# Optimization experiments

Hardware: AMD Instinct MI355X
Metric: run time of the kernel (lower is better)

The kernel has to match this reference:

```python
import jax, jax.numpy as jnp
import numpy as np

B, C1, C2, H, W, NH = 16, 256, 256, 64, 64, 8
C = C2 // 2          # hidden dim of retention blocks (c2*e)
HD = C // NH         # head dim
EPS = 1e-5           # torch BatchNorm2d / LayerNorm default eps


def _ln(x, g, b):
    mu = jnp.mean(x, -1, keepdims=True)
    var = jnp.mean((x - mu) ** 2, -1, keepdims=True)
    return (x - mu) * jax.lax.rsqrt(var + EPS) * g + b


def _bn_silu(y, g, b, m, v):
    # inference-mode BatchNorm2d (running stats) + SiLU, channels axis=1
    y = (y - m[:, None, None]) * jax.lax.rsqrt(v + EPS)[:, None, None] * g[:, None, None] + b[:, None, None]
    return jax.nn.silu(y)


def _decay1d(L, dec):
    # RelPos2d.generate_1d_decay: exp(decay_n * |i-j|), shape (NH, L, L)
    idx = jnp.arange(L)
    m = jnp.abs(idx[:, None] - idx[None, :]).astype(jnp.float32)
    return jnp.exp(dec[:, None, None] * m)


def setup_inputs() -> dict:
    key = jax.random.key(0)
    ks = jax.random.split(key, 8)
    s = 0.02
    return {
        'x': jax.random.normal(ks[0], (B, C1, H, W), jnp.float32),
        'cv1_w': jax.random.normal(ks[1], (2 * C, C1), jnp.float32) * s,
        'bn1_g': jnp.ones((2 * C,)), 'bn1_b': jnp.zeros((2 * C,)),
        'bn1_m': jnp.zeros((2 * C,)), 'bn1_v': jnp.ones((2 * C,)),
        'cv2_w': jax.random.normal(ks[2], (C2, 3 * C), jnp.float32) * s,
        'bn2_g': jnp.ones((C2,)), 'bn2_b': jnp.zeros((C2,)),
        'bn2_m': jnp.zeros((C2,)), 'bn2_v': jnp.ones((C2,)),
        'ln1_g': jnp.ones((C,)), 'ln1_b': jnp.zeros((C,)),
        'qkv_w': jax.random.normal(ks[3], (3 * C, C), jnp.float32) * s,
        'qkv_b': jnp.zeros((3 * C,)),
        'proj_w': jax.random.normal(ks[4], (C, C), jnp.float32) * s,
        'proj_b': jnp.zeros((C,)),
        'gamma': jnp.ones((C,)),
        'ln2_g': jnp.ones((C,)), 'ln2_b': jnp.zeros((C,)),
        'ffn_w1': jax.random.normal(ks[5], (2 * C, C), jnp.float32) * s,
        'ffn_b1': jnp.zeros((2 * C,)),
        'ffn_w2': jax.random.normal(ks[6], (C, 2 * C), jnp.float32) * s,
        'ffn_b2': jnp.zeros((C,)),
    }


def reference(x, cv1_w, bn1_g, bn1_b, bn1_m, bn1_v, cv2_w, bn2_g, bn2_b, bn2_m, bn2_v,
              ln1_g, ln1_b, qkv_w, qkv_b, proj_w, proj_b, gamma,
              ln2_g, ln2_b, ffn_w1, ffn_b1, ffn_w2, ffn_b2):
    # RelPos2d: decay per head, initial_value=2, heads_range=4; mode='chunk' -> 1D decays
    dec = jnp.log(1.0 - 2.0 ** (-2.0 - 4.0 * jnp.arange(NH, dtype=jnp.float32) / NH))
    decay_h = _decay1d(H, dec)  # (NH, H, H)
    decay_w = _decay1d(W, dec)  # (NH, W, W)

    # cv1: 1x1 conv + BN + SiLU, then chunk into two halves of C channels
    y = _bn_silu(jnp.einsum('bchw,oc->bohw', x, cv1_w), bn1_g, bn1_b, bn1_m, bn1_v)
    y1, y2 = y[:, :C], y[:, C:]

    # RetBlock on channels-last feature map
    f = jnp.transpose(y2, (0, 2, 3, 1))  # (B,H,W,C)
    res = f
    fn = _ln(f, ln1_g, ln1_b)
    qkv = fn @ qkv_w.T + qkv_b
    q, k, v = jnp.split(qkv, 3, axis=-1)

    def heads(t):
        return jnp.transpose(t.reshape(B, H, W, NH, HD), (0, 3, 1, 2, 4))  # (B,NH,H,W,HD)

    q, k, v = heads(q), heads(k), heads(v)

    # axial retention: row attention with exponential row-decay
    qk_h = jnp.einsum('bnhwc,bnHwc->bnhHw', q, k) * decay_h[None, :, :, :, None]
    out_h = jnp.einsum('bnhHw,bnHwc->bnhwc', qk_h, v)
    # column attention with exponential column-decay
    qk_w = jnp.einsum('bnhwc,bnhWc->bnhwW', q, k) * decay_w[None, :, None, :, :]
    out_w = jnp.einsum('bnhwW,bnhWc->bnhwc', qk_w, v)
    out = 0.5 * (out_h + out_w)
    out = jnp.transpose(out, (0, 2, 3, 1, 4)).reshape(B, H, W, C)

    f = res + (out @ proj_w.T + proj_b) * gamma
    res2 = f
    fn2 = _ln(f, ln2_g, ln2_b)
    h1 = jax.nn.gelu(fn2 @ ffn_w1.T + ffn_b1, approximate=False)
    f = res2 + (h1 @ ffn_w2.T + ffn_b2)

    f = jnp.transpose(f, (0, 3, 1, 2))  # back to (B,C,H,W)
    cat = jnp.concatenate([y1, y2, f], axis=1)  # (B,3C,H,W)
    return _bn_silu(jnp.einsum('bchw,oc->bohw', cat, cv2_w), bn2_g, bn2_b, bn2_m, bn2_v)
```

## Files before the change

kernel.cpp:

```cpp
#include <hip/hip_runtime.h>
#include <math.h>

#define LEPS 1e-5f
static constexpr int NPOS = 65536;

typedef __attribute__((ext_vector_type(8))) short short8;
typedef __attribute__((ext_vector_type(4))) float floatx4;

__device__ __forceinline__ ushort f2bf(float f) {
    unsigned int u = __float_as_uint(f);
    u += 0x7FFF + ((u >> 16) & 1);
    return (ushort)(u >> 16);
}
__device__ __forceinline__ float bfu(ushort h) {
    return __uint_as_float((unsigned int)h << 16);
}
__device__ __forceinline__ float bfl(unsigned int u) {
    return __uint_as_float(u << 16);
}
__device__ __forceinline__ float bfh(unsigned int u) {
    return __uint_as_float(u & 0xffff0000u);
}

struct WcvtArgs { const float* src[6]; ushort* dst[6]; int n[6]; };
__global__ __launch_bounds__(256)
void wcvt_k(WcvtArgs a)
{
    const int seg = blockIdx.y;
    const float* s = a.src[seg];
    ushort* d = a.dst[seg];
    const int n = a.n[seg];
    for (int i = blockIdx.x * 256 + threadIdx.x; i < n; i += gridDim.x * 256)
        d[i] = f2bf(s[i]);
}

__global__ __launch_bounds__(256)
void bnprep_k(const float* g1, const float* b1, const float* m1, const float* v1,
              const float* g2, const float* b2, const float* m2, const float* v2,
              float* s1, float* h1, float* s2, float* h2)
{
    const int i = threadIdx.x;
    if (blockIdx.x == 0) {
        const float s = g1[i] * rsqrtf(v1[i] + LEPS);
        s1[i] = s; h1[i] = b1[i] - m1[i] * s;
    } else {
        const float s = g2[i] * rsqrtf(v2[i] + LEPS);
        s2[i] = s; h2[i] = b2[i] - m2[i] * s;
    }
}

__global__ __launch_bounds__(256)
void tr_k(const float* __restrict__ x, ushort* __restrict__ xT)
{
    __shared__ float tile[64][65];
    const int t = threadIdx.x;
    const int bi = blockIdx.x;
    const int hwt = bi & 63, ct = (bi >> 6) & 3, b = bi >> 8;
    const int p0 = b * 4096 + hwt * 64, c0 = ct * 64;
    const float* src = x + ((size_t)(b * 256 + c0) << 12) + hwt * 64;
#pragma unroll
    for (int i = 0; i < 16; i++) {
        int cc = (t >> 6) + i * 4;
        tile[cc][t & 63] = src[((size_t)cc << 12) + (t & 63)];
    }
    __syncthreads();
    const int c2 = (t & 31) * 2;
    const int pr = t >> 5;
#pragma unroll
    for (int i = 0; i < 8; i++) {
        int pp = pr + i * 8;
        unsigned int u = (unsigned int)f2bf(tile[c2][pp])
                       | ((unsigned int)f2bf(tile[c2 + 1][pp]) << 16);
        *(unsigned int*)&xT[(size_t)(p0 + pp) * 256 + c0 + c2] = u;
    }
}

template<int KDIM, int ARS, int AMODE, int EPI, int LN>
__global__ __launch_bounds__(256)
void gemm_k(const ushort* __restrict__ A0, const ushort* __restrict__ A1,
            const ushort* __restrict__ Wm, const float* __restrict__ bias,
            const float* __restrict__ q0, const float* __restrict__ q1,
            const ushort* __restrict__ resh,
            const float* __restrict__ lng, const float* __restrict__ lnb,
            ushort* __restrict__ lnout, void* __restrict__ outv, int ors)
{
    __shared__ __align__(16) ushort smem[2 * 128 * 72];
    ushort (*As)[72] = (ushort (*)[72])smem;
    ushort (*Bs)[72] = (ushort (*)[72])(smem + 128 * 72);
    const int t = threadIdx.x;
    const int p0 = blockIdx.x * 128;
    const int o0 = blockIdx.y * 128;
    const int row = t >> 1, half = t & 1;
    const int lane = t & 63, wv = t >> 6;
    const int wm = (wv & 1) * 64, wn = (wv >> 1) * 64;
    const int ln15 = lane & 15, quad = lane >> 4;
    floatx4 acc[4][4] = {};

    for (int k0 = 0; k0 < KDIM; k0 += 64) {
        if (AMODE == 3) {
            const ushort* s1 = A0 + (size_t)(p0 + row) * 128 + k0 + half * 32;
            const ushort* s2 = A1 + (size_t)(p0 + row) * 128 + k0 + half * 32;
#pragma unroll
            for (int i = 0; i < 4; i++) {
                uint4 ua = ((const uint4*)s1)[i];
                uint4 ub = ((const uint4*)s2)[i];
                const unsigned int* ap = (const unsigned int*)&ua;
                const unsigned int* bp = (const unsigned int*)&ub;
                uint4 w;
                unsigned int* wp = (unsigned int*)&w;
#pragma unroll
                for (int j = 0; j < 4; j++)
                    wp[j] = (unsigned int)f2bf(0.5f * (bfl(ap[j]) + bfl(bp[j])))
                          | ((unsigned int)f2bf(0.5f * (bfh(ap[j]) + bfh(bp[j]))) << 16);
                *(uint4*)&As[row][half * 32 + i * 8] = w;
            }
        } else {
            const ushort* s;
            if (AMODE == 2) {
                if (k0 < 256) s = A0 + (size_t)(p0 + row) * 256 + k0 + half * 32;
                else          s = A1 + (size_t)(p0 + row) * 128 + (k0 - 256) + half * 32;
            } else {
                s = A0 + (size_t)(p0 + row) * ARS + k0 + half * 32;
            }
#pragma unroll
            for (int i = 0; i < 4; i++)
                *(uint4*)&As[row][half * 32 + i * 8] = ((const uint4*)s)[i];
        }
        {
            const ushort* s = Wm + (size_t)(o0 + row) * KDIM + k0 + half * 32;
#pragma unroll
            for (int i = 0; i < 4; i++)
                *(uint4*)&Bs[row][half * 32 + i * 8] = ((const uint4*)s)[i];
        }
        __syncthreads();
#pragma unroll
        for (int kc = 0; kc < 64; kc += 32) {
            short8 a[4], b[4];
#pragma unroll
            for (int i = 0; i < 4; i++)
                a[i] = *(const short8*)&As[wm + i * 16 + ln15][kc + quad * 8];
#pragma unroll
            for (int j = 0; j < 4; j++)
                b[j] = *(const short8*)&Bs[wn + j * 16 + ln15][kc + quad * 8];
#pragma unroll
            for (int i = 0; i < 4; i++)
#pragma unroll
                for (int j = 0; j < 4; j++)
                    acc[i][j] = __builtin_amdgcn_mfma_f32_16x16x32_bf16(
                        a[i], b[j], acc[i][j], 0, 0, 0);
        }
        __syncthreads();
    }

    if (EPI == 2) {
        float* cb = (float*)smem;
        float* ob = (float*)outv + (((size_t)(p0 >> 12) * 256) << 12);
        const int hw0 = p0 & 4095;
#pragma unroll
        for (int chunk = 0; chunk < 2; chunk++) {
            __syncthreads();
            if ((wn >> 6) == chunk) {
#pragma unroll
                for (int i = 0; i < 4; i++)
#pragma unroll
                for (int j = 0; j < 4; j++) {
                    const int ch = j * 16 + ln15;
                    const int o = o0 + chunk * 64 + ch;
                    const float sc = q0[o], sh = q1[o];
#pragma unroll
                    for (int r = 0; r < 4; r++) {
                        const int pos = wm + i * 16 + quad * 4 + r;
                        float v = acc[i][j][r] * sc + sh;
                        v = v / (1.f + __expf(-v));
                        cb[ch * 132 + pos] = v;
                    }
                }
            }
            __syncthreads();
#pragma unroll
            for (int it = 0; it < 8; it++) {
                const int flat = it * 1024 + t * 4;
                const int ch = flat >> 7, pos = flat & 127;
                const int o = o0 + chunk * 64 + ch;
                float4 v4 = *(const float4*)&cb[ch * 132 + pos];
                *(float4*)&ob[((size_t)o << 12) + hw0 + pos] = v4;
            }
        }
        return;
    }

    const bool lnact = LN && (EPI != 1 || o0 == 128);
    ushort (*lt)[136] = (ushort (*)[136])smem;
    ushort* o16 = (ushort*)outv;
#pragma unroll
    for (int i = 0; i < 4; i++) {
#pragma unroll
        for (int r = 0; r < 4; r++) {
            const int p = p0 + wm + i * 16 + quad * 4 + r;
#pragma unroll
            for (int j = 0; j < 4; j++) {
                const int ol = wn + j * 16 + ln15;
                const int o = o0 + ol;
                float v = acc[i][j][r];
                if (EPI == 0) {
                    v += bias[o];
                } else if (EPI == 1) {
                    v = v * q0[o] + q1[o];
                    v = v / (1.f + __expf(-v));
                } else if (EPI == 4) {
                    v = bfu(resh[(size_t)p * 256 + 128 + o]) + (v + bias[o]) * q0[o];
                }
                const ushort hv = f2bf(v);
                o16[(size_t)p * (size_t)ors + o] = hv;
                if (lnact) lt[p - p0][ol] = hv;
            }
        }
    }

    if (lnact) {
        __syncthreads();
        const int rrow = t >> 1, rhalf = t & 1;
        const ushort* rp = &lt[rrow][rhalf * 64];
        float s = 0.f, s2 = 0.f;
#pragma unroll
        for (int i = 0; i < 8; i++) {
            const uint4 u = *(const uint4*)(rp + i * 8);
            const unsigned int ww[4] = {u.x, u.y, u.z, u.w};
#pragma unroll
            for (int j = 0; j < 4; j++) {
                const float a = bfl(ww[j]), c = bfh(ww[j]);
                s += a + c; s2 += a * a + c * c;
            }
        }
        s += __shfl_xor(s, 1); s2 += __shfl_xor(s2, 1);
        const float mu = s * (1.f / 128.f);
        const float rn = rsqrtf(s2 * (1.f / 128.f) - mu * mu + LEPS);
        ushort* op = lnout + (size_t)(p0 + rrow) * 128 + rhalf * 64;
#pragma unroll
        for (int i = 0; i < 8; i++) {
            const uint4 u = *(const uint4*)(rp + i * 8);
            const unsigned int ww[4] = {u.x, u.y, u.z, u.w};
            uint4 wout;
            unsigned int* wo = (unsigned int*)&wout;
#pragma unroll
            for (int j = 0; j < 4; j++) {
                const int ch = rhalf * 64 + i * 8 + j * 2;
                const float2 gg = *(const float2*)(lng + ch);
                const float2 bb = *(const float2*)(lnb + ch);
                const float a = (bfl(ww[j]) - mu) * rn * gg.x + bb.x;
                const float c = (bfh(ww[j]) - mu) * rn * gg.y + bb.y;
                wo[j] = (unsigned int)f2bf(a) | ((unsigned int)f2bf(c) << 16);
            }
            *(uint4*)(op + i * 8) = wout;
        }
    }
}

__global__ __launch_bounds__(256)
void ffn_k(const ushort* __restrict__ fn2, const ushort* __restrict__ w1,
           const float* __restrict__ b1, const ushort* __restrict__ w2,
           const float* __restrict__ b2, ushort* __restrict__ f)
{
    __shared__ __align__(16) ushort smem[64 * 72 + 256 * 72 + 64 * 264];
    ushort (*Ax)[72]  = (ushort (*)[72])smem;
    ushort (*Wt)[72]  = (ushort (*)[72])(smem + 64 * 72);
    ushort (*H1)[264] = (ushort (*)[264])(smem + 64 * 72 + 256 * 72);
    const int t = threadIdx.x;
    const int p0 = blockIdx.x * 64;
    const int lane = t & 63, wv = t >> 6;
    const int ln15 = lane & 15, quad = lane >> 4;

    floatx4 acc1[4][4] = {};
    for (int k0 = 0; k0 < 128; k0 += 64) {
#pragma unroll
        for (int u = 0; u < 2; u++) {
            const int fi = t * 2 + u, r = fi >> 3, c = (fi & 7) * 8;
            *(uint4*)&Ax[r][c] = *(const uint4*)(fn2 + (size_t)(p0 + r) * 128 + k0 + c);
        }
#pragma unroll
        for (int u = 0; u < 8; u++)
            *(uint4*)&Wt[t][u * 8] = *(const uint4*)(w1 + (size_t)t * 128 + k0 + u * 8);
        __syncthreads();
#pragma unroll
        for (int kc = 0; kc < 64; kc += 32) {
            short8 a[4], b[4];
#pragma unroll
            for (int i = 0; i < 4; i++)
                a[i] = *(const short8*)&Ax[i * 16 + ln15][kc + quad * 8];
#pragma unroll
            for (int j = 0; j < 4; j++)
                b[j] = *(const short8*)&Wt[wv * 64 + j * 16 + ln15][kc + quad * 8];
#pragma unroll
            for (int i = 0; i < 4; i++)
#pragma unroll
                for (int j = 0; j < 4; j++)
                    acc1[i][j] = __builtin_amdgcn_mfma_f32_16x16x32_bf16(
                        a[i], b[j], acc1[i][j], 0, 0, 0);
        }
        __syncthreads();
    }
    {
        float bb1[4];
#pragma unroll
        for (int j = 0; j < 4; j++) bb1[j] = b1[wv * 64 + j * 16 + ln15];
#pragma unroll
        for (int i = 0; i < 4; i++)
#pragma unroll
        for (int j = 0; j < 4; j++)
#pragma unroll
        for (int r = 0; r < 4; r++) {
            float v = acc1[i][j][r] + bb1[j];
            v = 0.5f * v * (1.f + erff(v * 0.70710678118654752f));
            H1[i * 16 + quad * 4 + r][wv * 64 + j * 16 + ln15] = f2bf(v);
        }
    }
    __syncthreads();

    floatx4 acc2[4][2] = {};
    for (int k0 = 0; k0 < 256; k0 += 64) {
#pragma unroll
        for (int u = 0; u < 4; u++) {
            const int fi = t * 4 + u, r = fi >> 3, c = (fi & 7) * 8;
            *(uint4*)&Wt[r][c] = *(const uint4*)(w2 + (size_t)r * 256 + k0 + c);
        }
        __syncthreads();
#pragma unroll
        for (int kc = 0; kc < 64; kc += 32) {
            short8 a[4], b[2];
#pragma unroll
            for (int i = 0; i < 4; i++)
                a[i] = *(const short8*)&H1[i * 16 + ln15][k0 + kc + quad * 8];
#pragma unroll
            for (int j = 0; j < 2; j++)
                b[j] = *(const short8*)&Wt[wv * 32 + j * 16 + ln15][kc + quad * 8];
#pragma unroll
            for (int i = 0; i < 4; i++)
#pragma unroll
                for (int j = 0; j < 2; j++)
                    acc2[i][j] = __builtin_amdgcn_mfma_f32_16x16x32_bf16(
                        a[i], b[j], acc2[i][j], 0, 0, 0);
        }
        __syncthreads();
    }
    {
        float bb2[2];
#pragma unroll
        for (int j = 0; j < 2; j++) bb2[j] = b2[wv * 32 + j * 16 + ln15];
#pragma unroll
        for (int i = 0; i < 4; i++)
#pragma unroll
        for (int r = 0; r < 4; r++) {
            const size_t p = p0 + i * 16 + quad * 4 + r;
#pragma unroll
            for (int j = 0; j < 2; j++) {
                const int ch = wv * 32 + j * 16 + ln15;
                const size_t idx = p * 128 + ch;
                f[idx] = f2bf(bfu(f[idx]) + acc2[i][j][r] + bb2[j]);
            }
        }
    }
}

__global__ __launch_bounds__(256)
void attn_k(const ushort* __restrict__ qkv, ushort* __restrict__ oh,
            ushort* __restrict__ ow)
{
    __shared__ ushort VtS[4][16 * 72];
    __shared__ ushort SbS[4][64 * 72];
    __shared__ float dpow[128];
    const int t = threadIdx.x, wv = t >> 6, lane = t & 63;
    const int ln15 = lane & 15, quad = lane >> 4;
    const int dirH = (blockIdx.y == 0);
    ushort* outb = dirH ? oh : ow;
    const int blk = blockIdx.x;
    const int lg = blk & 15, n = (blk >> 4) & 7, b = blk >> 7;
    if (t < 128) {
        const float dec = logf(1.f - exp2f(-2.f - 0.5f * (float)n));
        int d = t - 63; if (d < 0) d = -d;
        dpow[t] = __expf(dec * (float)d);
    }
    const int fixed = lg * 4 + wv;
    const int stride = dirH ? 64 : 1;
    const size_t base = (size_t)b * 4096 + (dirH ? fixed : fixed * 64);
    const size_t cbase = base * 384 + n * 16;

    {
        const ushort* vp = qkv + cbase + (size_t)lane * stride * 384 + 256;
        const uint4 va = *(const uint4*)vp, vb = *(const uint4*)(vp + 8);
        ushort* vt = VtS[wv] + lane;
        const unsigned int w[8] = { va.x, va.y, va.z, va.w, vb.x, vb.y, vb.z, vb.w };
#pragma unroll
        for (int d = 0; d < 8; d++) {
            vt[(2 * d) * 72]     = (ushort)(w[d] & 0xffff);
            vt[(2 * d + 1) * 72] = (ushort)(w[d] >> 16);
        }
    }
    short8 qa[4], kb[4];
    {
        const short8 z = {0, 0, 0, 0, 0, 0, 0, 0};
#pragma unroll
        for (int mt = 0; mt < 4; mt++) {
            const int i = mt * 16 + ln15;
            if (quad < 2) {
                const ushort* qp = qkv + cbase + (size_t)i * stride * 384 + quad * 8;
                qa[mt] = *(const short8*)qp;
                kb[mt] = *(const short8*)(qp + 128);
            } else { qa[mt] = z; kb[mt] = z; }
        }
    }
    __syncthreads();

#pragma unroll
    for (int mt = 0; mt < 4; mt++) {
#pragma unroll
        for (int nt = 0; nt < 4; nt++) {
            floatx4 c = {0.f, 0.f, 0.f, 0.f};
            c = __builtin_amdgcn_mfma_f32_16x16x32_bf16(qa[mt], kb[nt], c, 0, 0, 0);
            const int i0 = mt * 16 + quad * 4;
            const int jl = nt * 16 + ln15;
            const float* lut = dpow + (i0 - jl + 63);
            ushort* sb = SbS[wv] + i0 * 72 + jl;
#pragma unroll
            for (int r = 0; r < 4; r++)
                sb[r * 72] = f2bf(c[r] * lut[r]);
        }
    }
    __syncthreads();

    short8 av[2];
#pragma unroll
    for (int c = 0; c < 2; c++)
        av[c] = *(const short8*)&VtS[wv][ln15 * 72 + c * 32 + quad * 8];
    floatx4 o[4] = {};
#pragma unroll
    for (int nt4 = 0; nt4 < 4; nt4++) {
#pragma unroll
        for (int c = 0; c < 2; c++) {
            const short8 bs = *(const short8*)
                &SbS[wv][(nt4 * 16 + ln15) * 72 + c * 32 + quad * 8];
            o[nt4] = __builtin_amdgcn_mfma_f32_16x16x32_bf16(av[c], bs, o[nt4], 0, 0, 0);
        }
    }
#pragma unroll
    for (int nt4 = 0; nt4 < 4; nt4++) {
        const int i = nt4 * 16 + ln15;
        ushort* op = outb + (base + (size_t)i * stride) * 128 + n * 16 + quad * 4;
        uint2 w;
        w.x = (unsigned int)f2bf(o[nt4][0]) | ((unsigned int)f2bf(o[nt4][1]) << 16);
        w.y = (unsigned int)f2bf(o[nt4][2]) | ((unsigned int)f2bf(o[nt4][3]) << 16);
        *(uint2*)op = w;
    }
}

extern "C" void kernel_launch(void* const* d_in, const int* in_sizes, int n_in,
                              void* d_out, int out_size, void* d_ws, size_t ws_size,
                              hipStream_t stream)
{
    const float* x      = (const float*)d_in[0];
    const float* cv1_w  = (const float*)d_in[1];
    const float* bn1_g  = (const float*)d_in[2];
    const float* bn1_b  = (const float*)d_in[3];
    const float* bn1_m  = (const float*)d_in[4];
    const float* bn1_v  = (const float*)d_in[5];
    const float* cv2_w  = (const float*)d_in[6];
    const float* bn2_g  = (const float*)d_in[7];
    const float* bn2_b  = (const float*)d_in[8];
    const float* bn2_m  = (const float*)d_in[9];
    const float* bn2_v  = (const float*)d_in[10];
    const float* ln1_g  = (const float*)d_in[11];
    const float* ln1_b  = (const float*)d_in[12];
    const float* qkv_w  = (const float*)d_in[13];
    const float* qkv_b  = (const float*)d_in[14];
    const float* proj_w = (const float*)d_in[15];
    const float* proj_b = (const float*)d_in[16];
    const float* gamma  = (const float*)d_in[17];
    const float* ln2_g  = (const float*)d_in[18];
    const float* ln2_b  = (const float*)d_in[19];
    const float* ffn_w1 = (const float*)d_in[20];
    const float* ffn_b1 = (const float*)d_in[21];
    const float* ffn_w2 = (const float*)d_in[22];
    const float* ffn_b2 = (const float*)d_in[23];

    ushort* W = (ushort*)d_ws;
    ushort* y    = W;
    ushort* f    = y    + (size_t)NPOS * 256;
    ushort* tmp  = f    + (size_t)NPOS * 128;
    ushort* owb  = tmp  + (size_t)NPOS * 128;
    ushort* qkvb = owb  + (size_t)NPOS * 128;
    ushort* xT   = qkvb + (size_t)NPOS * 384;
    ushort* wc1  = xT   + (size_t)NPOS * 256;
    ushort* wqkv = wc1  + 65536;
    ushort* wpr  = wqkv + 49152;
    ushort* ww1  = wpr  + 16384;
    ushort* ww2  = ww1  + 32768;
    ushort* wc2  = ww2  + 32768;
    float*  bns1 = (float*)(wc2 + 98304);
    float*  bnb1 = bns1 + 256;
    float*  bns2 = bnb1 + 256;
    float*  bnb2 = bns2 + 256;
    float*  out  = (float*)d_out;

    WcvtArgs wa;
    wa.src[0] = cv1_w;  wa.dst[0] = wc1;  wa.n[0] = 65536;
    wa.src[1] = qkv_w;  wa.dst[1] = wqkv; wa.n[1] = 49152;
    wa.src[2] = proj_w; wa.dst[2] = wpr;  wa.n[2] = 16384;
    wa.src[3] = ffn_w1; wa.dst[3] = ww1;  wa.n[3] = 32768;
    wa.src[4] = ffn_w2; wa.dst[4] = ww2;  wa.n[4] = 32768;
    wa.src[5] = cv2_w;  wa.dst[5] = wc2;  wa.n[5] = 98304;
    wcvt_k<<<dim3(96, 6), 256, 0, stream>>>(wa);
    bnprep_k<<<2, 256, 0, stream>>>(bn1_g, bn1_b, bn1_m, bn1_v,
                                    bn2_g, bn2_b, bn2_m, bn2_v,
                                    bns1, bnb1, bns2, bnb2);
    tr_k<<<4096, 256, 0, stream>>>(x, xT);

    gemm_k<256, 256, 0, 1, 1><<<dim3(512, 2), 256, 0, stream>>>(
        xT, nullptr, wc1, nullptr, bns1, bnb1, nullptr, ln1_g, ln1_b, tmp, y, 256);
    gemm_k<128, 128, 0, 0, 0><<<dim3(512, 3), 256, 0, stream>>>(
        tmp, nullptr, wqkv, qkv_b, nullptr, nullptr, nullptr, nullptr, nullptr,
        nullptr, qkvb, 384);
    attn_k<<<dim3(2048, 2), 256, 0, stream>>>(qkvb, tmp, owb);
    gemm_k<128, 128, 3, 4, 1><<<dim3(512, 1), 256, 0, stream>>>(
        tmp, owb, wpr, proj_b, gamma, nullptr, y, ln2_g, ln2_b, tmp, f, 128);
    ffn_k<<<1024, 256, 0, stream>>>(tmp, ww1, ffn_b1, ww2, ffn_b2, f);
    gemm_k<384, 0, 2, 2, 0><<<dim3(512, 2), 256, 0, stream>>>(
        y, f, wc2, nullptr, bns2, bnb2, nullptr, nullptr, nullptr, nullptr, out, 0);
}
```

Measured before the change: 367.5 us.

## Use direct global-to-LDS loads with XOR swizzle and staged coalesced epilogue stores

GEMM and FFN kernels now fill shared-memory tiles with global_load_lds 16-byte direct loads into an unpadded, XOR-swizzled layout, so the data no longer passes through registers. Fragment reads use the matching swizzle to avoid LDS bank conflicts. The bf16 epilogue writes go through an LDS tile first and are then stored as coalesced 16-byte rows. The FFN residual read-modify-write is also staged through LDS. Together these aim to cut VGPR pressure, instruction count and uncoalesced 2-byte global stores, at the cost of extra barriers and a dependence on the correctness of the swizzle and the direct-to-LDS builtin.

```diff
diff --git a/kernel.cpp b/kernel.cpp
--- a/kernel.cpp
+++ b/kernel.cpp
@@ -20,6 +20,12 @@
 }
 __device__ __forceinline__ float bfh(unsigned int u) {
     return __uint_as_float(u & 0xffff0000u);
+}
+
+typedef __attribute__((address_space(1))) const unsigned int gu32_t;
+typedef __attribute__((address_space(3))) unsigned int lu32_t;
+__device__ __forceinline__ void gld16(const ushort* g, ushort* l) {
+    __builtin_amdgcn_global_load_lds((gu32_t*)g, (lu32_t*)l, 16, 0, 0);
 }
 
 struct WcvtArgs { const float* src[6]; ushort* dst[6]; int n[6]; };
@@ -84,20 +90,24 @@
             const float* __restrict__ lng, const float* __restrict__ lnb,
             ushort* __restrict__ lnout, void* __restrict__ outv, int ors)
 {
-    __shared__ __align__(16) ushort smem[2 * 128 * 72];
-    ushort (*As)[72] = (ushort (*)[72])smem;
-    ushort (*Bs)[72] = (ushort (*)[72])(smem + 128 * 72);
+    __shared__ __align__(16) ushort smem[128 * 136];
+    ushort* As = smem;
+    ushort* Bs = smem + 128 * 64;
     const int t = threadIdx.x;
     const int p0 = blockIdx.x * 128;
     const int o0 = blockIdx.y * 128;
-    const int row = t >> 1, half = t & 1;
     const int lane = t & 63, wv = t >> 6;
     const int wm = (wv & 1) * 64, wn = (wv >> 1) * 64;
     const int ln15 = lane & 15, quad = lane >> 4;
+    const int dl_row = lane >> 3;
+    const int dl_sch = (lane & 7) ^ dl_row;
+    const int c_off0 = ((quad) ^ (ln15 & 7)) * 8;
+    const int c_off1 = ((4 + quad) ^ (ln15 & 7)) * 8;
     floatx4 acc[4][4] = {};
 
     for (int k0 = 0; k0 < KDIM; k0 += 64) {
         if (AMODE == 3) {
+            const int row = t >> 1, half = t & 1;
             const ushort* s1 = A0 + (size_t)(p0 + row) * 128 + k0 + half * 32;
             const ushort* s2 = A1 + (size_t)(p0 + row) * 128 + k0 + half * 32;
 #pragma unroll
@@ -112,36 +122,40 @@
                 for (int j = 0; j < 4; j++)
                     wp[j] = (unsigned int)f2bf(0.5f * (bfl(ap[j]) + bfl(bp[j])))
                           | ((unsigned int)f2bf(0.5f * (bfh(ap[j]) + bfh(bp[j]))) << 16);
-                *(uint4*)&As[row][half * 32 + i * 8] = w;
+                const int pch = (half * 4 + i) ^ (row & 7);
+                *(uint4*)&As[row * 64 + pch * 8] = w;
             }
         } else {
-            const ushort* s;
-            if (AMODE == 2) {
-                if (k0 < 256) s = A0 + (size_t)(p0 + row) * 256 + k0 + half * 32;
-                else          s = A1 + (size_t)(p0 + row) * 128 + (k0 - 256) + half * 32;
-            } else {
-                s = A0 + (size_t)(p0 + row) * ARS + k0 + half * 32;
-            }
+#pragma unroll
+            for (int i = 0; i < 4; i++) {
+                const int r0 = wv * 32 + i * 8;
+                const int row = r0 + dl_row;
+                const ushort* src;
+                if (AMODE == 2) {
+                    if (k0 < 256) src = A0 + (size_t)(p0 + row) * 256 + k0 + dl_sch * 8;
+                    else          src = A1 + (size_t)(p0 + row) * 128 + (k0 - 256) + dl_sch * 8;
+                } else {
+                    src = A0 + (size_t)(p0 + row) * ARS + k0 + dl_sch * 8;
+                }
+                gld16(src, &As[r0 * 64]);
+            }
+        }
+#pragma unroll
+        for (int i = 0; i < 4; i++) {
+            const int r0 = wv * 32 + i * 8;
+            gld16(Wm + (size_t)(o0 + r0 + dl_row) * KDIM + k0 + dl_sch * 8, &Bs[r0 * 64]);
+        }
+        __syncthreads();
+#pragma unroll
+        for (int kh = 0; kh < 2; kh++) {
+            const int co = kh ? c_off1 : c_off0;
+            short8 a[4], b[4];
 #pragma unroll
             for (int i = 0; i < 4; i++)
-                *(uint4*)&As[row][half * 32 + i * 8] = ((const uint4*)s)[i];
-        }
-        {
-            const ushort* s = Wm + (size_t)(o0 + row) * KDIM + k0 + half * 32;
-#pragma unroll
-            for (int i = 0; i < 4; i++)
-                *(uint4*)&Bs[row][half * 32 + i * 8] = ((const uint4*)s)[i];
-        }
-        __syncthreads();
-#pragma unroll
-        for (int kc = 0; kc < 64; kc += 32) {
-            short8 a[4], b[4];
-#pragma unroll
-            for (int i = 0; i < 4; i++)
-                a[i] = *(const short8*)&As[wm + i * 16 + ln15][kc + quad * 8];
+                a[i] = *(const short8*)&As[(wm + i * 16 + ln15) * 64 + co];
 #pragma unroll
             for (int j = 0; j < 4; j++)
-                b[j] = *(const short8*)&Bs[wn + j * 16 + ln15][kc + quad * 8];
+                b[j] = *(const short8*)&Bs[(wn + j * 16 + ln15) * 64 + co];
 #pragma unroll
             for (int i = 0; i < 4; i++)
 #pragma unroll
@@ -191,12 +205,12 @@
 
     const bool lnact = LN && (EPI != 1 || o0 == 128);
     ushort (*lt)[136] = (ushort (*)[136])smem;
-    ushort* o16 = (ushort*)outv;
 #pragma unroll
     for (int i = 0; i < 4; i++) {
 #pragma unroll
         for (int r = 0; r < 4; r++) {
-            const int p = p0 + wm + i * 16 + quad * 4 + r;
+            const int lr = wm + i * 16 + quad * 4 + r;
+            const int p = p0 + lr;
 #pragma unroll
             for (int j = 0; j < 4; j++) {
                 const int ol = wn + j * 16 + ln15;
@@ -210,15 +224,23 @@
                 } else if (EPI == 4) {
                     v = bfu(resh[(size_t)p * 256 + 128 + o]) + (v + bias[o]) * q0[o];
                 }
-                const ushort hv = f2bf(v);
-                o16[(size_t)p * (size_t)ors + o] = hv;
-                if (lnact) lt[p - p0][ol] = hv;
-            }
+                lt[lr][ol] = f2bf(v);
+            }
+        }
+    }
+    __syncthreads();
+    {
+        ushort* o16 = (ushort*)outv;
+#pragma unroll
+        for (int it = 0; it < 8; it++) {
+            const int flat = it * 256 + t;
+            const int row = flat >> 4, ch = (flat & 15) * 8;
+            *(uint4*)&o16[(size_t)(p0 + row) * (size_t)ors + o0 + ch] =
+                *(const uint4*)&lt[row][ch];
         }
     }
 
     if (lnact) {
-        __syncthreads();
         const int rrow = t >> 1, rhalf = t & 1;
         const ushort* rp = &lt[rrow][rhalf * 64];
         float s = 0.f, s2 = 0.f;
@@ -261,35 +283,42 @@
            const float* __restrict__ b1, const ushort* __restrict__ w2,
            const float* __restrict__ b2, ushort* __restrict__ f)
 {
-    __shared__ __align__(16) ushort smem[64 * 72 + 256 * 72 + 64 * 264];
-    ushort (*Ax)[72]  = (ushort (*)[72])smem;
-    ushort (*Wt)[72]  = (ushort (*)[72])(smem + 64 * 72);
-    ushort (*H1)[264] = (ushort (*)[264])(smem + 64 * 72 + 256 * 72);
+    __shared__ __align__(16) ushort smem[64 * 64 + 256 * 64 + 64 * 264];
+    ushort* Ax = smem;
+    ushort* Wt = smem + 64 * 64;
+    ushort (*H1)[264] = (ushort (*)[264])(smem + 64 * 64 + 256 * 64);
     const int t = threadIdx.x;
     const int p0 = blockIdx.x * 64;
     const int lane = t & 63, wv = t >> 6;
     const int ln15 = lane & 15, quad = lane >> 4;
+    const int dl_row = lane >> 3;
+    const int dl_sch = (lane & 7) ^ dl_row;
+    const int c_off0 = ((quad) ^ (ln15 & 7)) * 8;
+    const int c_off1 = ((4 + quad) ^ (ln15 & 7)) * 8;
 
     floatx4 acc1[4][4] = {};
     for (int k0 = 0; k0 < 128; k0 += 64) {
 #pragma unroll
-        for (int u = 0; u < 2; u++) {
-            const int fi = t * 2 + u, r = fi >> 3, c = (fi & 7) * 8;
-            *(uint4*)&Ax[r][c] = *(const uint4*)(fn2 + (size_t)(p0 + r) * 128 + k0 + c);
-        }
-#pragma unroll
-        for (int u = 0; u < 8; u++)
-            *(uint4*)&Wt[t][u * 8] = *(const uint4*)(w1 + (size_t)t * 128 + k0 + u * 8);
+        for (int i = 0; i < 2; i++) {
+            const int r0 = wv * 16 + i * 8;
+            gld16(fn2 + (size_t)(p0 + r0 + dl_row) * 128 + k0 + dl_sch * 8, &Ax[r0 * 64]);
+        }
+#pragma unroll
+        for (int i = 0; i < 8; i++) {
+            const int r0 = wv * 64 + i * 8;
+            gld16(w1 + (size_t)(r0 + dl_row) * 128 + k0 + dl_sch * 8, &Wt[r0 * 64]);
+        }
         __syncthreads();
 #pragma unroll
-        for (int kc = 0; kc < 64; kc += 32) {
+        for (int kh = 0; kh < 2; kh++) {
+            const int co = kh ? c_off1 : c_off0;
             short8 a[4], b[4];
 #pragma unroll
             for (int i = 0; i < 4; i++)
-                a[i] = *(const short8*)&Ax[i * 16 + ln15][kc + quad * 8];
+                a[i] = *(const short8*)&Ax[(i * 16 + ln15) * 64 + co];
 #pragma unroll
             for (int j = 0; j < 4; j++)
-                b[j] = *(const short8*)&Wt[wv * 64 + j * 16 + ln15][kc + quad * 8];
+                b[j] = *(const short8*)&Wt[(wv * 64 + j * 16 + ln15) * 64 + co];
 #pragma unroll
             for (int i = 0; i < 4; i++)
 #pragma unroll
@@ -319,20 +348,21 @@
     floatx4 acc2[4][2] = {};
     for (int k0 = 0; k0 < 256; k0 += 64) {
 #pragma unroll
-        for (int u = 0; u < 4; u++) {
-            const int fi = t * 4 + u, r = fi >> 3, c = (fi & 7) * 8;
-            *(uint4*)&Wt[r][c] = *(const uint4*)(w2 + (size_t)r * 256 + k0 + c);
+        for (int i = 0; i < 4; i++) {
+            const int r0 = wv * 32 + i * 8;
+            gld16(w2 + (size_t)(r0 + dl_row) * 256 + k0 + dl_sch * 8, &Wt[r0 * 64]);
         }
         __syncthreads();
 #pragma unroll
-        for (int kc = 0; kc < 64; kc += 32) {
+        for (int kh = 0; kh < 2; kh++) {
+            const int co = kh ? c_off1 : c_off0;
             short8 a[4], b[2];
 #pragma unroll
             for (int i = 0; i < 4; i++)
-                a[i] = *(const short8*)&H1[i * 16 + ln15][k0 + kc + quad * 8];
+                a[i] = *(const short8*)&H1[i * 16 + ln15][k0 + kh * 32 + quad * 8];
 #pragma unroll
             for (int j = 0; j < 2; j++)
-                b[j] = *(const short8*)&Wt[wv * 32 + j * 16 + ln15][kc + quad * 8];
+                b[j] = *(const short8*)&Wt[(wv * 32 + j * 16 + ln15) * 64 + co];
 #pragma unroll
             for (int i = 0; i < 4; i++)
 #pragma unroll
@@ -342,6 +372,14 @@
         }
         __syncthreads();
     }
+
+    ushort* Ft = smem;
+#pragma unroll
+    for (int i = 0; i < 4; i++) {
+        const int r0 = wv * 16 + i * 4;
+        gld16(f + (size_t)(p0 + r0 + (lane >> 4)) * 128 + (lane & 15) * 8, &Ft[r0 * 128]);
+    }
+    __syncthreads();
     {
         float bb2[2];
 #pragma unroll
@@ -350,14 +388,21 @@
         for (int i = 0; i < 4; i++)
 #pragma unroll
         for (int r = 0; r < 4; r++) {
-            const size_t p = p0 + i * 16 + quad * 4 + r;
+            const int pos = i * 16 + quad * 4 + r;
 #pragma unroll
             for (int j = 0; j < 2; j++) {
                 const int ch = wv * 32 + j * 16 + ln15;
-                const size_t idx = p * 128 + ch;
-                f[idx] = f2bf(bfu(f[idx]) + acc2[i][j][r] + bb2[j]);
-            }
-        }
+                const int idx = pos * 128 + ch;
+                Ft[idx] = f2bf(bfu(Ft[idx]) + acc2[i][j][r] + bb2[j]);
+            }
+        }
+    }
+    __syncthreads();
+#pragma unroll
+    for (int it = 0; it < 4; it++) {
+        const int flat = it * 256 + t;
+        const int row = flat >> 4, ch = (flat & 15) * 8;
+        *(uint4*)&f[(size_t)(p0 + row) * 128 + ch] = *(const uint4*)&Ft[row * 128 + ch];
     }
 }
 
```

Result: faster. 355.7 us (-3.2%).
